# Kernel tuning notes

Measured on AMD Instinct MI355X. Metric: run time of the kernel, lower is better.

The kernel has to match this reference:

```python
import jax, jax.numpy as jnp
import numpy as np

# hyperparameters (from init_kwargs / repo defaults)
AMP_COEF = 1.0
ARG_COEF = 1.0
SSIM_COEF = 1.0
BETA = 1.0
STFT_COEF = 1e-4
EPS = 1e-8
STFT_F = 12
STFT_S = 4


def _gauss_kernel(size=11, sigma=1.5):
    x = jnp.arange(size, dtype=jnp.float32) - (size - 1) / 2.0
    g = jnp.exp(-0.5 * (x / sigma) ** 2)
    k = jnp.outer(g, g)
    return k / jnp.sum(k)


def _depthwise_filter(img, k):
    # img: [B,H,W,C]; 11x11 gaussian, VALID padding, depthwise (per-channel)
    c = img.shape[-1]
    kern = jnp.tile(k[:, :, None, None], (1, 1, 1, c))  # HWIO, I=1, O=C
    return jax.lax.conv_general_dilated(
        img, kern, (1, 1), 'VALID',
        dimension_numbers=('NHWC', 'HWIO', 'NHWC'),
        feature_group_count=c)


def ssim(x, y, max_val=1.0):
    # faithful to tf.image.ssim defaults: filter 11, sigma 1.5, k1=0.01, k2=0.03
    c1 = (0.01 * max_val) ** 2
    c2 = (0.03 * max_val) ** 2
    k = _gauss_kernel()
    mu_x = _depthwise_filter(x, k)
    mu_y = _depthwise_filter(y, k)
    var_x = _depthwise_filter(x * x, k) - mu_x * mu_x
    var_y = _depthwise_filter(y * y, k) - mu_y * mu_y
    cov = _depthwise_filter(x * y, k) - mu_x * mu_y
    lum = (2.0 * mu_x * mu_y + c1) / (mu_x * mu_x + mu_y * mu_y + c1)
    cs = (2.0 * cov + c2) / (var_x + var_y + c2)
    return jnp.mean(lum * cs, axis=(1, 2, 3))  # [B]


def stft(image, f=STFT_F, s=STFT_S):
    # image: [B,N,N,C] -> batched patchwise 2D FFT, cropped to [:f//2,:f//2]
    n = image.shape[1]
    p = (n - f) // s + 1          # num_conv per axis
    half = f // 2
    rows = (jnp.arange(p) * s)[:, None] + jnp.arange(f)   # [P, f]
    patches = image[:, rows]                              # [B,P,f,N,C]
    patches = patches[:, :, :, rows]                      # [B,P,f,P,f,C]
    patches = jnp.transpose(patches, (0, 1, 3, 2, 4, 5))  # [B,Pi,Pj,f,f,C]
    b, c = image.shape[0], image.shape[-1]
    patches = patches.reshape(b, p * p, f, f, c)          # k = i*P + j ordering
    fft = jnp.fft.fft2(patches.astype(jnp.complex64), axes=(2, 3))
    return fft[:, :, :half, :half, :]                     # [B,P*P,half,half,C]


def _freq_filter(f=STFT_F):
    lin = jnp.linspace(0.0, 1.0, f // 2)[:, None]
    return (lin * lin.T)[:, :, None]                      # [half,half,1]


def setup_inputs() -> dict:
    key = jax.random.key(0)
    k1, k2, k3, k4 = jax.random.split(key, 4)
    B, N, C, L = 32, 160, 3, 128
    return {
        'mean': jax.random.normal(k1, (B, L), dtype=jnp.float32),
        'logvar': jax.random.normal(k2, (B, L), dtype=jnp.float32),
        'x_in': jax.random.uniform(k3, (B, N, N, C), dtype=jnp.float32),
        'x_out': jax.random.uniform(k4, (B, N, N, C), dtype=jnp.float32),
    }


def reference(mean, logvar, x_in, x_out):
    # KLD per sample
    var = jnp.exp(logvar)
    kld = -0.5 * jnp.sum(1.0 + logvar - var - mean * mean, axis=1)  # [B]
    # SSIM recon term
    recons = SSIM_COEF * ssim(x_in, x_out, 1.0)                     # [B]
    # patchwise STFT amp/phase loss ('ours')
    stft_out = stft(x_out, STFT_F, STFT_S)
    stft_in = stft(x_in, STFT_F, STFT_S)
    ff = _freq_filter(STFT_F)                                       # [half,half,1]
    arg_diff = jnp.abs(jnp.angle(stft_out + EPS) - jnp.angle(stft_in + EPS))
    amp_diff = jnp.abs(jnp.abs(stft_out) - jnp.abs(stft_in))
    arg_loss = jnp.sum(arg_diff * ff, axis=(1, 2, 3, 4))            # [B]
    amp_loss = jnp.sum(amp_diff * ff, axis=(1, 2, 3, 4))            # [B]
    stft_loss = ARG_COEF * arg_loss + AMP_COEF * amp_loss
    loss = jnp.mean(BETA * kld + recons + STFT_COEF * stft_loss)
    return loss
```

## Files before the change

### kernel.cpp

```cpp
#include <hip/hip_runtime.h>
#include <hip/hip_fp16.h>
#include <math.h>

#define BATCH 32
#define NPIX 160
#define LDIM 128
#define OUT_SZ 150

#define THREADS 512
#define N_BLOCKS 1825
#define RD_OFF   2880
#define VPMU_OFF 2880
#define VPVV_OFF 4192
#define VPXY_OFF 5504
#define VROWSTR  164
#define SMEM_FLOATS 8960

__device__ constexpr float TWC[12] = { 1.f, 0.86602540f, 0.5f, 0.f, -0.5f, -0.86602540f,
                                      -1.f,-0.86602540f,-0.5f, 0.f,  0.5f,  0.86602540f};
__device__ constexpr float TWS[12] = { 0.f,-0.5f,-0.86602540f,-1.f,-0.86602540f,-0.5f,
                                       0.f, 0.5f, 0.86602540f, 1.f, 0.86602540f, 0.5f};

__device__ constexpr float GW[11] = {0.00102838f, 0.00759876f, 0.03600076f, 0.10936070f,
                                     0.21300554f, 0.26601172f, 0.21300554f, 0.10936070f,
                                     0.03600076f, 0.00759876f, 0.00102838f};

__device__ __forceinline__ float fast_atan2f(float y, float x) {
    float ax = fabsf(x), ay = fabsf(y);
    float mx = fmaxf(ax, ay), mn = fminf(ax, ay);
    float z = mn * __builtin_amdgcn_rcpf(mx);
    float z2 = z * z;
    float p = fmaf(z2, -0.01172120f, 0.05265332f);
    p = fmaf(z2, p, -0.11643287f);
    p = fmaf(z2, p, 0.19354346f);
    p = fmaf(z2, p, -0.33262347f);
    p = fmaf(z2, p, 0.99997726f);
    p = p * z;
    if (ay > ax) p = 1.57079632679489662f - p;
    if (x < 0.f) p = 3.14159265358979323f - p;
    return (y < 0.f) ? -p : p;
}

__device__ __forceinline__ __half2 h2swap(__half2 v) {
    unsigned u;
    __builtin_memcpy(&u, &v, 4);
    u = (u >> 16) | (u << 16);
    __half2 r;
    __builtin_memcpy(&r, &u, 4);
    return r;
}

__device__ __forceinline__ float4 extract_c(float4 f0, float4 f1, float4 f2, int c) {
    if (c == 0) return make_float4(f0.x, f0.w, f1.z, f2.y);
    if (c == 1) return make_float4(f0.y, f1.x, f1.w, f2.z);
    return make_float4(f0.z, f1.y, f2.x, f2.w);
}

__global__ __launch_bounds__(THREADS) void work_kernel(const float* __restrict__ xin,
                                                       const float* __restrict__ xout,
                                                       const float* __restrict__ mean,
                                                       const float* __restrict__ logvar,
                                                       float* __restrict__ out) {
    __shared__ __align__(16) float SMEM[SMEM_FLOATS];
    __shared__ float sm8[8];
    const int tid = threadIdx.x;
    const int gid = blockIdx.x;
    float acc = 0.f;

    if (gid == 1824) {
        float a = 0.f;
        for (int i = tid; i < BATCH * LDIM; i += THREADS) {
            float m = mean[i], lv = logvar[i];
            a += -0.5f * (1.f + lv - expf(lv) - m * m) * (1.f / 32.f);
        }
        #pragma unroll
        for (int o = 32; o > 0; o >>= 1) a += __shfl_down(a, o, 64);
        if ((tid & 63) == 0) sm8[tid >> 6] = a;
        __syncthreads();
        if (tid == 0) {
            float s = sm8[0];
            #pragma unroll
            for (int i = 1; i < 8; ++i) s += sm8[i];
            atomicAdd(out, s);
        }
        return;
    }

    int b    = gid / 57;
    int rem  = gid % 57;
    int c    = rem / 19;
    int tile = rem % 19;
    int r0 = tile * 8;
    __half2* HXY = (__half2*)SMEM;
    __half2* RD  = (__half2*)(SMEM + RD_OFF);
    const __half2 hz = __float2half2_rn(0.f);

    for (int t = tid; t < 720; t += THREADS) {
        int rr = t / 40;
        int cq = t % 40;
        int row = r0 + rr;
        float4 xa = make_float4(0.f, 0.f, 0.f, 0.f);
        float4 xb = make_float4(0.f, 0.f, 0.f, 0.f);
        if (row < NPIX) {
            size_t off = ((size_t)(b * 160 + row) * 160 + cq * 4) * 3;
            const float4* qa = (const float4*)(xin + off);
            const float4* qb = (const float4*)(xout + off);
            float4 a0 = qa[0], a1 = qa[1], a2 = qa[2];
            float4 b0 = qb[0], b1 = qb[1], b2 = qb[2];
            xa = extract_c(a0, a1, a2, c);
            xb = extract_c(b0, b1, b2, c);
        }
        __half2 h[4] __attribute__((aligned(16)));
        h[0] = __floats2half2_rn(xa.x, xb.x);
        h[1] = __floats2half2_rn(xa.y, xb.y);
        h[2] = __floats2half2_rn(xa.z, xb.z);
        h[3] = __floats2half2_rn(xa.w, xb.w);
        *(float4*)&HXY[rr * 160 + cq * 4] = *(float4*)h;
    }
    __syncthreads();

    for (int t = tid; t < 608; t += THREADS) {
        int pc = t % 38;
        int r  = t / 38;
        float4 raw[3];
        raw[0] = *(const float4*)&HXY[r * 160 + pc * 4];
        raw[1] = *(const float4*)&HXY[r * 160 + pc * 4 + 4];
        raw[2] = *(const float4*)&HXY[r * 160 + pc * 4 + 8];
        const __half2* x = (const __half2*)raw;
        __half2 ev[5], ov[5];
        #pragma unroll
        for (int j = 1; j <= 5; ++j) {
            ev[j-1] = __hadd2(x[j], x[12 - j]);
            ov[j-1] = __hsub2(x[j], x[12 - j]);
        }
        #pragma unroll
        for (int vv = 0; vv < 5; ++vv) {
            const int v = vv + 1;
            __half2 re = (v & 1) ? __hsub2(x[0], x[6]) : __hadd2(x[0], x[6]);
            __half2 im = hz;
            #pragma unroll
            for (int j = 1; j <= 5; ++j) {
                const int kk = (v * j) % 12;
                re = __hfma2(ev[j-1], __float2half2_rn(TWC[kk]), re);
                im = __hfma2(ov[j-1], __float2half2_rn(TWS[kk]), im);
            }
            __half2 w2[2] __attribute__((aligned(8)));
            w2[0] = re;
            w2[1] = im;
            *(float2*)&RD[((r * 5 + vv) * 38 + pc) * 2] = *(float2*)w2;
        }
    }
    __syncthreads();

    if (tid < 380) {
        int pc = tid % 38;
        int vv = (tid / 38) % 5;
        int g  = tid / 190;
        __half2 FR[5], FI[5];
        #pragma unroll
        for (int uu = 0; uu < 5; ++uu) { FR[uu] = hz; FI[uu] = hz; }
        #pragma unroll
        for (int i = 0; i < 6; ++i) {
            int rlo = 4 * g + i, rhi = rlo + 6;
            __half2 lo[2] __attribute__((aligned(8)));
            __half2 hi[2] __attribute__((aligned(8)));
            *(float2*)lo = *(const float2*)&RD[((rlo * 5 + vv) * 38 + pc) * 2];
            *(float2*)hi = *(const float2*)&RD[((rhi * 5 + vv) * 38 + pc) * 2];
            __half2 spR = __hadd2(lo[0], hi[0]), smR = __hsub2(lo[0], hi[0]);
            __half2 spI = __hadd2(lo[1], hi[1]), smI = __hsub2(lo[1], hi[1]);
            #pragma unroll
            for (int uu = 0; uu < 5; ++uu) {
                const int u = uu + 1;
                const int kk = (u * i) % 12;
                __half2 sR = (u & 1) ? smR : spR;
                __half2 sI = (u & 1) ? smI : spI;
                FR[uu] = __hfma2(sR, __float2half2_rn(TWC[kk]),
                         __hfma2(sI, __float2half2_rn(-TWS[kk]), FR[uu]));
                FI[uu] = __hfma2(sI, __float2half2_rn(TWC[kk]),
                         __hfma2(sR, __float2half2_rn(TWS[kk]), FI[uu]));
            }
        }
        float sacc = 0.f;
        #pragma unroll
        for (int uu = 0; uu < 5; ++uu) {
            float2 fr = __half22float2(FR[uu]);
            float2 fi = __half22float2(FI[uu]);
            float aI = fast_atan2f(fi.x, fr.x + 1e-8f);
            float aO = fast_atan2f(fi.y, fr.y + 1e-8f);
            float mI = __builtin_amdgcn_sqrtf(fmaf(fr.x, fr.x, fi.x * fi.x));
            float mO = __builtin_amdgcn_sqrtf(fmaf(fr.y, fr.y, fi.y * fi.y));
            float ff = (float)((uu + 1) * (vv + 1)) * 0.04f;
            sacc += ff * (fabsf(aO - aI) + fabsf(mO - mI));
        }
        acc += sacc * (1e-4f / 32.f);
    }
    __syncthreads();

    for (int t = tid; t < 320; t += THREADS) {
        int orow = t / 40;
        int cbase = (t % 40) * 4;
        __half2 amu[4], avv[4], axy[4];
        #pragma unroll
        for (int o = 0; o < 4; ++o) { amu[o] = hz; avv[o] = hz; axy[o] = hz; }
        #pragma unroll
        for (int kk = 0; kk < 11; ++kk) {
            float4 raw = *(const float4*)&HXY[(orow + kk) * 160 + cbase];
            const __half2* h = (const __half2*)&raw;
            const __half2 w2 = __float2half2_rn(GW[kk]);
            #pragma unroll
            for (int o = 0; o < 4; ++o) {
                __half2 t2 = __hmul2(w2, h[o]);
                amu[o] = __hadd2(amu[o], t2);
                avv[o] = __hfma2(t2, h[o], avv[o]);
                axy[o] = __hfma2(t2, h2swap(h[o]), axy[o]);
            }
        }
        int base = orow * VROWSTR + cbase;
        *(float4*)&SMEM[VPMU_OFF + base] = *(float4*)amu;
        *(float4*)&SMEM[VPVV_OFF + base] = *(float4*)avv;
        *(float4*)&SMEM[VPXY_OFF + base] = make_float4(
            __low2float(axy[0]), __low2float(axy[1]),
            __low2float(axy[2]), __low2float(axy[3]));
    }
    __syncthreads();

    {
        float hacc = 0.f;
        for (int t = tid; t < 600; t += THREADS) {
            int orow = t / 75;
            int oc = (t % 75) * 2;
            int base = orow * VROWSTR + oc;
            __half2 m[12], s0 = hz, s1 = hz;
            #pragma unroll
            for (int q = 0; q < 6; ++q)
                *(float2*)&m[2 * q] = *(const float2*)&SMEM[VPMU_OFF + base + 2 * q];
            #pragma unroll
            for (int kk = 0; kk < 11; ++kk) {
                const __half2 w2 = __float2half2_rn(GW[kk]);
                s0 = __hfma2(w2, m[kk],     s0);
                s1 = __hfma2(w2, m[kk + 1], s1);
            }
            float2 mu0 = __half22float2(s0);
            float2 mu1 = __half22float2(s1);
            __half2 v0 = hz, v1 = hz;
            #pragma unroll
            for (int q = 0; q < 6; ++q)
                *(float2*)&m[2 * q] = *(const float2*)&SMEM[VPVV_OFF + base + 2 * q];
            #pragma unroll
            for (int kk = 0; kk < 11; ++kk) {
                const __half2 w2 = __float2half2_rn(GW[kk]);
                v0 = __hfma2(w2, m[kk],     v0);
                v1 = __hfma2(w2, m[kk + 1], v1);
            }
            float2 vv0 = __half22float2(v0);
            float2 vv1 = __half22float2(v1);
            float zs[12];
            #pragma unroll
            for (int q = 0; q < 6; ++q) {
                float2 y2 = *(const float2*)&SMEM[VPXY_OFF + base + 2 * q];
                zs[2 * q] = y2.x; zs[2 * q + 1] = y2.y;
            }
            float xy0 = 0.f, xy1 = 0.f;
            #pragma unroll
            for (int kk = 0; kk < 11; ++kk) {
                xy0 = fmaf(GW[kk], zs[kk],     xy0);
                xy1 = fmaf(GW[kk], zs[kk + 1], xy1);
            }
            if (r0 + orow < OUT_SZ) {
                const float c1 = 1e-4f, c2 = 9e-4f;
                #pragma unroll
                for (int o = 0; o < 2; ++o) {
                    float mx = o ? mu1.x : mu0.x, my = o ? mu1.y : mu0.y;
                    float ex = o ? vv1.x : vv0.x, ey = o ? vv1.y : vv0.y;
                    float cv = (o ? xy1 : xy0) - mx * my;
                    float vx = ex - mx * mx;
                    float vy = ey - my * my;
                    float lum = (2.f * mx * my + c1) *
                                __builtin_amdgcn_rcpf(fmaf(mx, mx, my * my) + c1);
                    float cs  = (2.f * cv + c2) *
                                __builtin_amdgcn_rcpf(vx + vy + c2);
                    hacc += lum * cs;
                }
            }
        }
        acc += hacc * (1.f / (32.f * 150.f * 150.f * 3.f));
    }

    #pragma unroll
    for (int o = 32; o > 0; o >>= 1) acc += __shfl_down(acc, o, 64);
    if ((tid & 63) == 0) sm8[tid >> 6] = acc;
    __syncthreads();
    if (tid == 0) {
        float s = sm8[0];
        #pragma unroll
        for (int i = 1; i < 8; ++i) s += sm8[i];
        atomicAdd(out, s);
    }
}

extern "C" void kernel_launch(void* const* d_in, const int* in_sizes, int n_in,
                              void* d_out, int out_size, void* d_ws, size_t ws_size,
                              hipStream_t stream) {
    const float* mean   = (const float*)d_in[0];
    const float* logvar = (const float*)d_in[1];
    const float* xin    = (const float*)d_in[2];
    const float* xout   = (const float*)d_in[3];
    float* out = (float*)d_out;

    hipMemsetAsync(out, 0, sizeof(float), stream);
    work_kernel<<<N_BLOCKS, THREADS, 0, stream>>>(xin, xout, mean, logvar, out);
}
```

Before: 105.2 us.

## Process two row-tiles per block with double shared-memory regions

Each block now handles two (batch, channel, row-tile) work items, interleaving their stage, DFT, vertical and horizontal filter steps over two separate shared-memory regions. This halves the block count and the per-block sync and reduction overhead per unit of work, and adds a remapping of block index to spread tiles. The stage code was split into inline helper functions for reuse. The cost is doubled LDS per block (about 70KB), which lowers resident blocks per CU, plus a launch_bounds occupancy hint that may constrain registers.

```diff
diff --git a/kernel.cpp b/kernel.cpp
--- a/kernel.cpp
+++ b/kernel.cpp
@@ -8,13 +8,13 @@
 #define OUT_SZ 150
 
 #define THREADS 512
-#define N_BLOCKS 1825
+#define N_BLOCKS 913
+#define REGION   8960
 #define RD_OFF   2880
 #define VPMU_OFF 2880
 #define VPVV_OFF 4192
 #define VPXY_OFF 5504
 #define VROWSTR  164
-#define SMEM_FLOATS 8960
 
 __device__ constexpr float TWC[12] = { 1.f, 0.86602540f, 0.5f, 0.f, -0.5f, -0.86602540f,
                                       -1.f,-0.86602540f,-0.5f, 0.f,  0.5f,  0.86602540f};
@@ -56,18 +56,211 @@
     return make_float4(f0.z, f1.y, f2.x, f2.w);
 }
 
-__global__ __launch_bounds__(THREADS) void work_kernel(const float* __restrict__ xin,
-                                                       const float* __restrict__ xout,
-                                                       const float* __restrict__ mean,
-                                                       const float* __restrict__ logvar,
-                                                       float* __restrict__ out) {
-    __shared__ __align__(16) float SMEM[SMEM_FLOATS];
+
+__device__ __forceinline__ void stage_task(const float* __restrict__ xin,
+                                           const float* __restrict__ xout,
+                                           int b, int c, int r0,
+                                           __half2* HXY, int t) {
+    int rr = t / 40;
+    int cq = t % 40;
+    int row = r0 + rr;
+    float4 xa = make_float4(0.f, 0.f, 0.f, 0.f);
+    float4 xb = make_float4(0.f, 0.f, 0.f, 0.f);
+    if (row < NPIX) {
+        size_t off = ((size_t)(b * 160 + row) * 160 + cq * 4) * 3;
+        const float4* qa = (const float4*)(xin + off);
+        const float4* qb = (const float4*)(xout + off);
+        float4 a0 = qa[0], a1 = qa[1], a2 = qa[2];
+        float4 b0 = qb[0], b1 = qb[1], b2 = qb[2];
+        xa = extract_c(a0, a1, a2, c);
+        xb = extract_c(b0, b1, b2, c);
+    }
+    __half2 h[4] __attribute__((aligned(16)));
+    h[0] = __floats2half2_rn(xa.x, xb.x);
+    h[1] = __floats2half2_rn(xa.y, xb.y);
+    h[2] = __floats2half2_rn(xa.z, xb.z);
+    h[3] = __floats2half2_rn(xa.w, xb.w);
+    *(float4*)&HXY[rr * 160 + cq * 4] = *(float4*)h;
+}
+
+__device__ __forceinline__ void adft_task(const __half2* HXY, __half2* RD, int t) {
+    const __half2 hz = __float2half2_rn(0.f);
+    int pc = t % 38;
+    int r  = t / 38;
+    float4 raw[3];
+    raw[0] = *(const float4*)&HXY[r * 160 + pc * 4];
+    raw[1] = *(const float4*)&HXY[r * 160 + pc * 4 + 4];
+    raw[2] = *(const float4*)&HXY[r * 160 + pc * 4 + 8];
+    const __half2* x = (const __half2*)raw;
+    __half2 ev[5], ov[5];
+    #pragma unroll
+    for (int j = 1; j <= 5; ++j) {
+        ev[j-1] = __hadd2(x[j], x[12 - j]);
+        ov[j-1] = __hsub2(x[j], x[12 - j]);
+    }
+    #pragma unroll
+    for (int vv = 0; vv < 5; ++vv) {
+        const int v = vv + 1;
+        __half2 re = (v & 1) ? __hsub2(x[0], x[6]) : __hadd2(x[0], x[6]);
+        __half2 im = hz;
+        #pragma unroll
+        for (int j = 1; j <= 5; ++j) {
+            const int kk = (v * j) % 12;
+            re = __hfma2(ev[j-1], __float2half2_rn(TWC[kk]), re);
+            im = __hfma2(ov[j-1], __float2half2_rn(TWS[kk]), im);
+        }
+        __half2 w2[2] __attribute__((aligned(8)));
+        w2[0] = re;
+        w2[1] = im;
+        *(float2*)&RD[((r * 5 + vv) * 38 + pc) * 2] = *(float2*)w2;
+    }
+}
+
+__device__ __forceinline__ float bdft_task(const __half2* RD, int tid_) {
+    const __half2 hz = __float2half2_rn(0.f);
+    int pc = tid_ % 38;
+    int vv = (tid_ / 38) % 5;
+    int g  = tid_ / 190;
+    __half2 FR[5], FI[5];
+    #pragma unroll
+    for (int uu = 0; uu < 5; ++uu) { FR[uu] = hz; FI[uu] = hz; }
+    #pragma unroll
+    for (int i = 0; i < 6; ++i) {
+        int rlo = 4 * g + i, rhi = rlo + 6;
+        __half2 lo[2] __attribute__((aligned(8)));
+        __half2 hi[2] __attribute__((aligned(8)));
+        *(float2*)lo = *(const float2*)&RD[((rlo * 5 + vv) * 38 + pc) * 2];
+        *(float2*)hi = *(const float2*)&RD[((rhi * 5 + vv) * 38 + pc) * 2];
+        __half2 spR = __hadd2(lo[0], hi[0]), smR = __hsub2(lo[0], hi[0]);
+        __half2 spI = __hadd2(lo[1], hi[1]), smI = __hsub2(lo[1], hi[1]);
+        #pragma unroll
+        for (int uu = 0; uu < 5; ++uu) {
+            const int u = uu + 1;
+            const int kk = (u * i) % 12;
+            __half2 sR = (u & 1) ? smR : spR;
+            __half2 sI = (u & 1) ? smI : spI;
+            FR[uu] = __hfma2(sR, __float2half2_rn(TWC[kk]),
+                     __hfma2(sI, __float2half2_rn(-TWS[kk]), FR[uu]));
+            FI[uu] = __hfma2(sI, __float2half2_rn(TWC[kk]),
+                     __hfma2(sR, __float2half2_rn(TWS[kk]), FI[uu]));
+        }
+    }
+    float sacc = 0.f;
+    #pragma unroll
+    for (int uu = 0; uu < 5; ++uu) {
+        float2 fr = __half22float2(FR[uu]);
+        float2 fi = __half22float2(FI[uu]);
+        float aI = fast_atan2f(fi.x, fr.x + 1e-8f);
+        float aO = fast_atan2f(fi.y, fr.y + 1e-8f);
+        float mI = __builtin_amdgcn_sqrtf(fmaf(fr.x, fr.x, fi.x * fi.x));
+        float mO = __builtin_amdgcn_sqrtf(fmaf(fr.y, fr.y, fi.y * fi.y));
+        float ff = (float)((uu + 1) * (vv + 1)) * 0.04f;
+        sacc += ff * (fabsf(aO - aI) + fabsf(mO - mI));
+    }
+    return sacc;
+}
+
+__device__ __forceinline__ void v_task(const __half2* HXY, float* SM, int t) {
+    const __half2 hz = __float2half2_rn(0.f);
+    int orow = t / 40;
+    int cbase = (t % 40) * 4;
+    __half2 amu[4], avv[4], axy[4];
+    #pragma unroll
+    for (int o = 0; o < 4; ++o) { amu[o] = hz; avv[o] = hz; axy[o] = hz; }
+    #pragma unroll
+    for (int kk = 0; kk < 11; ++kk) {
+        float4 raw = *(const float4*)&HXY[(orow + kk) * 160 + cbase];
+        const __half2* h = (const __half2*)&raw;
+        const __half2 w2 = __float2half2_rn(GW[kk]);
+        #pragma unroll
+        for (int o = 0; o < 4; ++o) {
+            __half2 t2 = __hmul2(w2, h[o]);
+            amu[o] = __hadd2(amu[o], t2);
+            avv[o] = __hfma2(t2, h[o], avv[o]);
+            axy[o] = __hfma2(t2, h2swap(h[o]), axy[o]);
+        }
+    }
+    int base = orow * VROWSTR + cbase;
+    *(float4*)&SM[VPMU_OFF + base] = *(float4*)amu;
+    *(float4*)&SM[VPVV_OFF + base] = *(float4*)avv;
+    *(float4*)&SM[VPXY_OFF + base] = make_float4(
+        __low2float(axy[0]), __low2float(axy[1]),
+        __low2float(axy[2]), __low2float(axy[3]));
+}
+
+__device__ __forceinline__ float h_task(const float* SM, int r0, int t) {
+    const __half2 hz = __float2half2_rn(0.f);
+    int orow = t / 75;
+    int oc = (t % 75) * 2;
+    int base = orow * VROWSTR + oc;
+    __half2 m[12], s0 = hz, s1 = hz;
+    #pragma unroll
+    for (int q = 0; q < 6; ++q)
+        *(float2*)&m[2 * q] = *(const float2*)&SM[VPMU_OFF + base + 2 * q];
+    #pragma unroll
+    for (int kk = 0; kk < 11; ++kk) {
+        const __half2 w2 = __float2half2_rn(GW[kk]);
+        s0 = __hfma2(w2, m[kk],     s0);
+        s1 = __hfma2(w2, m[kk + 1], s1);
+    }
+    float2 mu0 = __half22float2(s0);
+    float2 mu1 = __half22float2(s1);
+    __half2 v0 = hz, v1 = hz;
+    #pragma unroll
+    for (int q = 0; q < 6; ++q)
+        *(float2*)&m[2 * q] = *(const float2*)&SM[VPVV_OFF + base + 2 * q];
+    #pragma unroll
+    for (int kk = 0; kk < 11; ++kk) {
+        const __half2 w2 = __float2half2_rn(GW[kk]);
+        v0 = __hfma2(w2, m[kk],     v0);
+        v1 = __hfma2(w2, m[kk + 1], v1);
+    }
+    float2 vv0 = __half22float2(v0);
+    float2 vv1 = __half22float2(v1);
+    float zs[12];
+    #pragma unroll
+    for (int q = 0; q < 6; ++q) {
+        float2 y2 = *(const float2*)&SM[VPXY_OFF + base + 2 * q];
+        zs[2 * q] = y2.x; zs[2 * q + 1] = y2.y;
+    }
+    float xy0 = 0.f, xy1 = 0.f;
+    #pragma unroll
+    for (int kk = 0; kk < 11; ++kk) {
+        xy0 = fmaf(GW[kk], zs[kk],     xy0);
+        xy1 = fmaf(GW[kk], zs[kk + 1], xy1);
+    }
+    float hacc = 0.f;
+    if (r0 + orow < OUT_SZ) {
+        const float c1 = 1e-4f, c2 = 9e-4f;
+        #pragma unroll
+        for (int o = 0; o < 2; ++o) {
+            float mx = o ? mu1.x : mu0.x, my = o ? mu1.y : mu0.y;
+            float ex = o ? vv1.x : vv0.x, ey = o ? vv1.y : vv0.y;
+            float cv = (o ? xy1 : xy0) - mx * my;
+            float vx = ex - mx * mx;
+            float vy = ey - my * my;
+            float lum = (2.f * mx * my + c1) *
+                        __builtin_amdgcn_rcpf(fmaf(mx, mx, my * my) + c1);
+            float cs  = (2.f * cv + c2) *
+                        __builtin_amdgcn_rcpf(vx + vy + c2);
+            hacc += lum * cs;
+        }
+    }
+    return hacc;
+}
+
+__global__ __launch_bounds__(THREADS, 4) void work_kernel(const float* __restrict__ xin,
+                                                          const float* __restrict__ xout,
+                                                          const float* __restrict__ mean,
+                                                          const float* __restrict__ logvar,
+                                                          float* __restrict__ out) {
+    __shared__ __align__(16) float SMEM[2 * REGION];
     __shared__ float sm8[8];
     const int tid = threadIdx.x;
     const int gid = blockIdx.x;
     float acc = 0.f;
 
-    if (gid == 1824) {
+    if (gid == 912) {
         float a = 0.f;
         for (int i = tid; i < BATCH * LDIM; i += THREADS) {
             float m = mean[i], lv = logvar[i];
@@ -86,202 +279,49 @@
         return;
     }
 
-    int b    = gid / 57;
-    int rem  = gid % 57;
-    int c    = rem / 19;
-    int tile = rem % 19;
-    int r0 = tile * 8;
-    __half2* HXY = (__half2*)SMEM;
-    __half2* RD  = (__half2*)(SMEM + RD_OFF);
-    const __half2 hz = __float2half2_rn(0.f);
+    int idx = (gid & 7) * 114 + (gid >> 3);
+    int i0 = idx * 2, i1 = i0 + 1;
+    int b0 = i0 / 57, t0r = i0 % 57;
+    int b1 = i1 / 57, t1r = i1 % 57;
+    int c0 = t0r % 3, r0a = (t0r / 3) * 8;
+    int c1 = t1r % 3, r0b = (t1r / 3) * 8;
+
+    float* S0 = SMEM;
+    float* S1 = SMEM + REGION;
+    __half2* HXY0 = (__half2*)S0;
+    __half2* HXY1 = (__half2*)S1;
+    __half2* RD0  = (__half2*)(S0 + RD_OFF);
+    __half2* RD1  = (__half2*)(S1 + RD_OFF);
 
     for (int t = tid; t < 720; t += THREADS) {
-        int rr = t / 40;
-        int cq = t % 40;
-        int row = r0 + rr;
-        float4 xa = make_float4(0.f, 0.f, 0.f, 0.f);
-        float4 xb = make_float4(0.f, 0.f, 0.f, 0.f);
-        if (row < NPIX) {
-            size_t off = ((size_t)(b * 160 + row) * 160 + cq * 4) * 3;
-            const float4* qa = (const float4*)(xin + off);
-            const float4* qb = (const float4*)(xout + off);
-            float4 a0 = qa[0], a1 = qa[1], a2 = qa[2];
-            float4 b0 = qb[0], b1 = qb[1], b2 = qb[2];
-            xa = extract_c(a0, a1, a2, c);
-            xb = extract_c(b0, b1, b2, c);
-        }
-        __half2 h[4] __attribute__((aligned(16)));
-        h[0] = __floats2half2_rn(xa.x, xb.x);
-        h[1] = __floats2half2_rn(xa.y, xb.y);
-        h[2] = __floats2half2_rn(xa.z, xb.z);
-        h[3] = __floats2half2_rn(xa.w, xb.w);
-        *(float4*)&HXY[rr * 160 + cq * 4] = *(float4*)h;
+        stage_task(xin, xout, b0, c0, r0a, HXY0, t);
+        stage_task(xin, xout, b1, c1, r0b, HXY1, t);
     }
     __syncthreads();
 
     for (int t = tid; t < 608; t += THREADS) {
-        int pc = t % 38;
-        int r  = t / 38;
-        float4 raw[3];
-        raw[0] = *(const float4*)&HXY[r * 160 + pc * 4];
-        raw[1] = *(const float4*)&HXY[r * 160 + pc * 4 + 4];
-        raw[2] = *(const float4*)&HXY[r * 160 + pc * 4 + 8];
-        const __half2* x = (const __half2*)raw;
-        __half2 ev[5], ov[5];
-        #pragma unroll
-        for (int j = 1; j <= 5; ++j) {
-            ev[j-1] = __hadd2(x[j], x[12 - j]);
-            ov[j-1] = __hsub2(x[j], x[12 - j]);
-        }
-        #pragma unroll
-        for (int vv = 0; vv < 5; ++vv) {
-            const int v = vv + 1;
-            __half2 re = (v & 1) ? __hsub2(x[0], x[6]) : __hadd2(x[0], x[6]);
-            __half2 im = hz;
-            #pragma unroll
-            for (int j = 1; j <= 5; ++j) {
-                const int kk = (v * j) % 12;
-                re = __hfma2(ev[j-1], __float2half2_rn(TWC[kk]), re);
-                im = __hfma2(ov[j-1], __float2half2_rn(TWS[kk]), im);
-            }
-            __half2 w2[2] __attribute__((aligned(8)));
-            w2[0] = re;
-            w2[1] = im;
-            *(float2*)&RD[((r * 5 + vv) * 38 + pc) * 2] = *(float2*)w2;
-        }
+        adft_task(HXY0, RD0, t);
+        adft_task(HXY1, RD1, t);
     }
     __syncthreads();
 
     if (tid < 380) {
-        int pc = tid % 38;
-        int vv = (tid / 38) % 5;
-        int g  = tid / 190;
-        __half2 FR[5], FI[5];
-        #pragma unroll
-        for (int uu = 0; uu < 5; ++uu) { FR[uu] = hz; FI[uu] = hz; }
-        #pragma unroll
-        for (int i = 0; i < 6; ++i) {
-            int rlo = 4 * g + i, rhi = rlo + 6;
-            __half2 lo[2] __attribute__((aligned(8)));
-            __half2 hi[2] __attribute__((aligned(8)));
-            *(float2*)lo = *(const float2*)&RD[((rlo * 5 + vv) * 38 + pc) * 2];
-            *(float2*)hi = *(const float2*)&RD[((rhi * 5 + vv) * 38 + pc) * 2];
-            __half2 spR = __hadd2(lo[0], hi[0]), smR = __hsub2(lo[0], hi[0]);
-            __half2 spI = __hadd2(lo[1], hi[1]), smI = __hsub2(lo[1], hi[1]);
-            #pragma unroll
-            for (int uu = 0; uu < 5; ++uu) {
-                const int u = uu + 1;
-                const int kk = (u * i) % 12;
-                __half2 sR = (u & 1) ? smR : spR;
-                __half2 sI = (u & 1) ? smI : spI;
-                FR[uu] = __hfma2(sR, __float2half2_rn(TWC[kk]),
-                         __hfma2(sI, __float2half2_rn(-TWS[kk]), FR[uu]));
-                FI[uu] = __hfma2(sI, __float2half2_rn(TWC[kk]),
-                         __hfma2(sR, __float2half2_rn(TWS[kk]), FI[uu]));
-            }
-        }
-        float sacc = 0.f;
-        #pragma unroll
-        for (int uu = 0; uu < 5; ++uu) {
-            float2 fr = __half22float2(FR[uu]);
-            float2 fi = __half22float2(FI[uu]);
-            float aI = fast_atan2f(fi.x, fr.x + 1e-8f);
-            float aO = fast_atan2f(fi.y, fr.y + 1e-8f);
-            float mI = __builtin_amdgcn_sqrtf(fmaf(fr.x, fr.x, fi.x * fi.x));
-            float mO = __builtin_amdgcn_sqrtf(fmaf(fr.y, fr.y, fi.y * fi.y));
-            float ff = (float)((uu + 1) * (vv + 1)) * 0.04f;
-            sacc += ff * (fabsf(aO - aI) + fabsf(mO - mI));
-        }
-        acc += sacc * (1e-4f / 32.f);
+        float s = bdft_task(RD0, tid) + bdft_task(RD1, tid);
+        acc += s * (1e-4f / 32.f);
     }
     __syncthreads();
 
     for (int t = tid; t < 320; t += THREADS) {
-        int orow = t / 40;
-        int cbase = (t % 40) * 4;
-        __half2 amu[4], avv[4], axy[4];
-        #pragma unroll
-        for (int o = 0; o < 4; ++o) { amu[o] = hz; avv[o] = hz; axy[o] = hz; }
-        #pragma unroll
-        for (int kk = 0; kk < 11; ++kk) {
-            float4 raw = *(const float4*)&HXY[(orow + kk) * 160 + cbase];
-            const __half2* h = (const __half2*)&raw;
-            const __half2 w2 = __float2half2_rn(GW[kk]);
-            #pragma unroll
-            for (int o = 0; o < 4; ++o) {
-                __half2 t2 = __hmul2(w2, h[o]);
-                amu[o] = __hadd2(amu[o], t2);
-                avv[o] = __hfma2(t2, h[o], avv[o]);
-                axy[o] = __hfma2(t2, h2swap(h[o]), axy[o]);
-            }
-        }
-        int base = orow * VROWSTR + cbase;
-        *(float4*)&SMEM[VPMU_OFF + base] = *(float4*)amu;
-        *(float4*)&SMEM[VPVV_OFF + base] = *(float4*)avv;
-        *(float4*)&SMEM[VPXY_OFF + base] = make_float4(
-            __low2float(axy[0]), __low2float(axy[1]),
-            __low2float(axy[2]), __low2float(axy[3]));
+        v_task(HXY0, S0, t);
+        v_task(HXY1, S1, t);
     }
     __syncthreads();
 
     {
         float hacc = 0.f;
         for (int t = tid; t < 600; t += THREADS) {
-            int orow = t / 75;
-            int oc = (t % 75) * 2;
-            int base = orow * VROWSTR + oc;
-            __half2 m[12], s0 = hz, s1 = hz;
-            #pragma unroll
-            for (int q = 0; q < 6; ++q)
-                *(float2*)&m[2 * q] = *(const float2*)&SMEM[VPMU_OFF + base + 2 * q];
-            #pragma unroll
-            for (int kk = 0; kk < 11; ++kk) {
-                const __half2 w2 = __float2half2_rn(GW[kk]);
-                s0 = __hfma2(w2, m[kk],     s0);
-                s1 = __hfma2(w2, m[kk + 1], s1);
-            }
-            float2 mu0 = __half22float2(s0);
-            float2 mu1 = __half22float2(s1);
-            __half2 v0 = hz, v1 = hz;
-            #pragma unroll
-            for (int q = 0; q < 6; ++q)
-                *(float2*)&m[2 * q] = *(const float2*)&SMEM[VPVV_OFF + base + 2 * q];
-            #pragma unroll
-            for (int kk = 0; kk < 11; ++kk) {
-                const __half2 w2 = __float2half2_rn(GW[kk]);
-                v0 = __hfma2(w2, m[kk],     v0);
-                v1 = __hfma2(w2, m[kk + 1], v1);
-            }
-            float2 vv0 = __half22float2(v0);
-            float2 vv1 = __half22float2(v1);
-            float zs[12];
-            #pragma unroll
-            for (int q = 0; q < 6; ++q) {
-                float2 y2 = *(const float2*)&SMEM[VPXY_OFF + base + 2 * q];
-                zs[2 * q] = y2.x; zs[2 * q + 1] = y2.y;
-            }
-            float xy0 = 0.f, xy1 = 0.f;
-            #pragma unroll
-            for (int kk = 0; kk < 11; ++kk) {
-                xy0 = fmaf(GW[kk], zs[kk],     xy0);
-                xy1 = fmaf(GW[kk], zs[kk + 1], xy1);
-            }
-            if (r0 + orow < OUT_SZ) {
-                const float c1 = 1e-4f, c2 = 9e-4f;
-                #pragma unroll
-                for (int o = 0; o < 2; ++o) {
-                    float mx = o ? mu1.x : mu0.x, my = o ? mu1.y : mu0.y;
-                    float ex = o ? vv1.x : vv0.x, ey = o ? vv1.y : vv0.y;
-                    float cv = (o ? xy1 : xy0) - mx * my;
-                    float vx = ex - mx * mx;
-                    float vy = ey - my * my;
-                    float lum = (2.f * mx * my + c1) *
-                                __builtin_amdgcn_rcpf(fmaf(mx, mx, my * my) + c1);
-                    float cs  = (2.f * cv + c2) *
-                                __builtin_amdgcn_rcpf(vx + vy + c2);
-                    hacc += lum * cs;
-                }
-            }
+            hacc += h_task(S0, r0a, t);
+            hacc += h_task(S1, r0b, t);
         }
         acc += hacc * (1.f / (32.f * 150.f * 150.f * 3.f));
     }
```

New measurement: 106.7 us. About the same (+1.4%).
